# Kernel tuning notes

Measured on AMD Instinct MI355X. Metric: run time of the kernel, lower is better.

## Reference

```python
import jax, jax.numpy as jnp
import numpy as np

DT = 0.5
NE, NIN = 400, 784
# excitatory LIF
THRESH_E, OFFSET, VRESET_E, EREST_E, REFRAC_E, TAU_MEM_E = -52.0, 20.0, -65.0, -65.0, 5.0, 100.0
# inhibitory LIF
THRESH_I, VRESET_I, EREST_I, REFRAC_I, TAU_MEM_I = -40.0, -45.0, -60.0, 2.0, 10.0
# synapses
TAU_SYN_E, TAU_SYN_I = 1.0, 2.0
E_EI, E_IE, E_EE = 0.0, -100.0, 0.0
# STDP
TC_P1, TC_P2, TC_PRE = 20.0, 40.0, 20.0
NU_PRE, NU_POST, WMAX = 0.0001, 0.01, 1.0
THETA0 = 20.0


def lif_step(mem, rc, I, thresh, v_reset, erest, tau, refrac):
    # conductance-based LIF with refractory period (inferred LIFei semantics)
    active = rc <= 0.0
    mem = jnp.where(active, mem + (erest - mem + I) * (DT / tau), mem)
    rc = jnp.maximum(rc - DT, 0.0)
    spike = (active & (mem > thresh)).astype(mem.dtype)
    fired = spike > 0.0
    mem = jnp.where(fired, v_reset, mem)
    rc = jnp.where(fired, refrac, rc)
    return mem, rc, spike


def setup_inputs() -> dict:
    key = jax.random.key(0)
    k1, k2 = jax.random.split(key)
    x = jax.random.uniform(k1, (50, 512, NIN), dtype=jnp.float32)  # Poisson-rate encoded frames
    W_ine = (jax.random.uniform(k2, (NE, NIN), dtype=jnp.float32) + 0.01) * 0.3  # create_ine
    W_ei = jnp.eye(NE, dtype=jnp.float32) * 10.4                                  # create_ei
    W_ie = (jnp.ones((NE, NE), jnp.float32) - jnp.eye(NE, dtype=jnp.float32)) * 17.0  # create_ie
    return {"x": x, "W_ine": W_ine, "W_ei": W_ei, "W_ie": W_ie}


def reference(x, W_ine, W_ei, W_ie):
    T, B, _ = x.shape
    z_e = jnp.zeros((B, NE), x.dtype)

    def step(carry, xt_t):
        xt, t = xt_t
        (W, g_ine, g_ei, g_ie, Iie, mem_e, rc_e, mem_i, rc_i,
         theta, tr_pre, tp1, tp2) = carry
        # normweight: rows sum to 78.4
        W = W / (jnp.sum(W, axis=1, keepdims=True) / 78.4)
        # input -> e synapse (STDP-plastic)
        dg_ine = xt @ W.T                         # (B, NE)
        I_ine = g_ine * (E_EE - mem_e)            # g=0 at t=0 -> I=0 (matches None init)
        g_ine = g_ine + (dg_ine - g_ine) * (DT / TAU_SYN_E)
        # excitatory LIF with adaptive threshold
        thr_e = THRESH_E - OFFSET + theta
        mem_e, rc_e, spike_e = lif_step(mem_e, rc_e, I_ine + Iie, thr_e,
                                        VRESET_E, EREST_E, TAU_MEM_E, REFRAC_E)
        # e -> i synapse
        dg_ei = spike_e @ W_ei.T
        I_ei = g_ei * (E_EI - mem_i)
        g_ei = g_ei + (dg_ei - g_ei) * (DT / TAU_SYN_E)
        # inhibitory LIF
        mem_i, rc_i, spike_i = lif_step(mem_i, rc_i, I_ei, THRESH_I,
                                        VRESET_I, EREST_I, TAU_MEM_I, REFRAC_I)
        # i -> e synapse (current fed into NEXT step's lif_e)
        dg_ie = spike_i @ W_ie.T
        Iie = g_ie * (E_IE - mem_e)
        g_ie = g_ie + (dg_ie - g_ie) * (DT / TAU_SYN_I)
        # threshold homeostasis
        theta = theta * (1.0 - DT / 1e7) + 0.05 * spike_e
        # pre trace: first call copies x, later decay then set to 1 where x>0.9
        tr_pre_upd = jnp.where(xt > 0.9, 1.0, tr_pre * (1.0 - DT / TC_PRE))
        tr_pre = jnp.where(t == 0, xt, tr_pre_upd)
        # post traces: return decayed value, then set to 1 where spike
        ret1 = tp1 * (1.0 - DT / TC_P1)
        ret2 = tp2 * (1.0 - DT / TC_P2)
        fired = spike_e > 0.9
        tp1 = jnp.where(fired, 1.0, ret1)
        tp2 = jnp.where(fired, 1.0, ret2)
        # STDP: autograd.grad of dg=x@W^T w.r.t. W with grad_outputs G is G^T @ x
        dw = (NU_PRE * jnp.einsum('be,bi->ei', ret1, xt)
              + NU_POST * jnp.einsum('be,bi->ei', spike_e * ret2, tr_pre))
        W = jnp.clip(W + dw, 0.0, WMAX)
        new_carry = (W, g_ine, g_ei, g_ie, Iie, mem_e, rc_e, mem_i, rc_i,
                     theta, tr_pre, tp1, tp2)
        return new_carry, spike_e

    carry0 = (W_ine,
              z_e, z_e, z_e,                      # g_ine, g_ei, g_ie
              z_e,                                # Iie
              jnp.full((B, NE), EREST_E, x.dtype), z_e,   # mem_e, rc_e
              jnp.full((B, NE), EREST_I, x.dtype), z_e,   # mem_i, rc_i
              jnp.full((B, NE), THETA0, x.dtype),         # theta
              jnp.zeros((B, NIN), x.dtype),               # trace_pre
              z_e, z_e)                                   # trace_post1/2
    _, spikes = jax.lax.scan(step, carry0, (x, jnp.arange(T)))
    return spikes  # (T, B, NE)
```

## Files before the change

kernel.cpp:

```cpp
#include <hip/hip_runtime.h>

#define NE 400
#define NIN 784
#define BB 512
#define TT 50

#define KC1 7
#define KCH1 112
#define KC2 4
#define KCH2 128

constexpr float C_KE     = (float)(0.5 / 100.0);
constexpr float C_KI     = (float)(0.5 / 10.0);
constexpr float C_GSE    = 0.5f;
constexpr float C_GSI    = 0.25f;
constexpr float C_DECTH  = (float)(1.0 - 0.5 / 1e7);
constexpr float C_DEC1   = (float)(1.0 - 0.5 / 20.0);
constexpr float C_DEC2   = (float)(1.0 - 0.5 / 40.0);
constexpr float C_DECPRE = (float)(1.0 - 0.5 / 20.0);
constexpr float C_NUPRE  = (float)0.0001;
constexpr float C_NUPOST = 0.01f;

__global__ void k_init(float* g_ine, float* g_ei, float* g_ie, float* Iie,
                       float* mem_e, float* rc_e, float* mem_i, float* rc_i,
                       float* theta, float* tp1, float* tp2) {
    int i = blockIdx.x * blockDim.x + threadIdx.x;
    if (i < BB * NE) {
        g_ine[i] = 0.f; g_ei[i] = 0.f; g_ie[i] = 0.f; Iie[i] = 0.f;
        mem_e[i] = -65.0f; rc_e[i] = 0.f;
        mem_i[i] = -60.0f; rc_i[i] = 0.f;
        theta[i] = 20.0f; tp1[i] = 0.f; tp2[i] = 0.f;
    }
}

__global__ __launch_bounds__(256) void k_rowsum0(const float* __restrict__ W,
                                                 float* __restrict__ d) {
    int e = blockIdx.x, tid = threadIdx.x;
    __shared__ float red[256];
    float s = 0.f;
    if (tid < 196) {
        float4 w = *(const float4*)&W[e * NIN + tid * 4];
        s = w.x + w.y + w.z + w.w;
    }
    red[tid] = s;
    __syncthreads();
    for (int off = 128; off > 0; off >>= 1) {
        if (tid < off) red[tid] += red[tid + off];
        __syncthreads();
    }
    if (tid == 0) d[e] = red[0] / 78.4f;
}

__global__ __launch_bounds__(256) void k_gemm1(const float* __restrict__ x,
                                               const float* __restrict__ W,
                                               float* __restrict__ dgp) {
    __shared__ float xs[16][68];
    __shared__ float ws[16][68];
    int tx = threadIdx.x & 15, ty = threadIdx.x >> 4;
    int lid = threadIdx.x;
    int e0 = blockIdx.x * 64, b0 = blockIdx.y * 64;
    int kbase = blockIdx.z * KCH1;

    float acc[4][4];
#pragma unroll
    for (int r = 0; r < 4; r++)
#pragma unroll
        for (int c = 0; c < 4; c++) acc[r][c] = 0.f;

    for (int kt = 0; kt < KCH1; kt += 16) {
        int k0 = kbase + kt;
        {
            int r = lid >> 2, cb = (lid & 3) * 4;
            float4 xv = *(const float4*)&x[(b0 + r) * NIN + k0 + cb];
            xs[cb + 0][r] = xv.x; xs[cb + 1][r] = xv.y;
            xs[cb + 2][r] = xv.z; xs[cb + 3][r] = xv.w;
            float4 wv;
            if (e0 + r < NE) wv = *(const float4*)&W[(e0 + r) * NIN + k0 + cb];
            else wv = make_float4(0.f, 0.f, 0.f, 0.f);
            ws[cb + 0][r] = wv.x; ws[cb + 1][r] = wv.y;
            ws[cb + 2][r] = wv.z; ws[cb + 3][r] = wv.w;
        }
        __syncthreads();
#pragma unroll
        for (int k = 0; k < 16; k++) {
            float4 av = *(const float4*)&xs[k][ty * 4];
            float4 bv = *(const float4*)&ws[k][tx * 4];
            float a[4] = {av.x, av.y, av.z, av.w};
            float b[4] = {bv.x, bv.y, bv.z, bv.w};
#pragma unroll
            for (int r = 0; r < 4; r++)
#pragma unroll
                for (int c = 0; c < 4; c++) acc[r][c] += a[r] * b[c];
        }
        __syncthreads();
    }
    if (e0 + tx * 4 < NE) {
        float* base = dgp + (size_t)blockIdx.z * BB * NE;
#pragma unroll
        for (int r = 0; r < 4; r++) {
            float4 v = make_float4(acc[r][0], acc[r][1], acc[r][2], acc[r][3]);
            *(float4*)&base[(b0 + ty * 4 + r) * NE + e0 + tx * 4] = v;
        }
    }
}

__global__ __launch_bounds__(512) void k_mid(const float* __restrict__ dgp,
                                             const float* __restrict__ d,
                                             const float* __restrict__ xt,
                                             float* __restrict__ tr, int t,
                                             float* g_ine, float* g_ei, float* g_ie,
                                             float* Iie, float* mem_e, float* rc_e,
                                             float* mem_i, float* rc_i, float* theta,
                                             float* tp1, float* tp2,
                                             float* __restrict__ A1,
                                             float* __restrict__ A2,
                                             float* __restrict__ out_t) {
    if (blockIdx.x >= BB) {
        int base = (blockIdx.x - BB) * 2048 + threadIdx.x * 4;
        float4 xv = *(const float4*)&xt[base];
        float4 o;
        if (t == 0) {
            o = xv;
        } else {
            float4 tv = *(const float4*)&tr[base];
            o.x = (xv.x > 0.9f) ? 1.0f : tv.x * C_DECPRE;
            o.y = (xv.y > 0.9f) ? 1.0f : tv.y * C_DECPRE;
            o.z = (xv.z > 0.9f) ? 1.0f : tv.z * C_DECPRE;
            o.w = (xv.w > 0.9f) ? 1.0f : tv.w * C_DECPRE;
        }
        *(float4*)&tr[base] = o;
        return;
    }
    int b = blockIdx.x;
    int e = threadIdx.x;
    __shared__ float red[512];
    int idx = b * NE + e;

    float spk_i = 0.f, spk_e = 0.f;
    float g1 = 0.f, me = 0.f, re = 0.f, th = 0.f, g2 = 0.f, mi = 0.f, ri = 0.f;

    if (e < NE) {
        float dg = 0.f;
#pragma unroll
        for (int c = 0; c < KC1; c++) dg += dgp[(size_t)c * BB * NE + idx];
        dg = dg / d[e];
        g1 = g_ine[idx]; me = mem_e[idx]; re = rc_e[idx];
        th = theta[idx];
        float Ii = Iie[idx];
        float I_in = g1 * (0.0f - me);
        g1 = g1 + (dg - g1) * C_GSE;
        bool act = (re <= 0.0f);
        float I = I_in + Ii;
        if (act) me = me + ((-65.0f - me) + I) * C_KE;
        re = fmaxf(re - 0.5f, 0.0f);
        float thr = -72.0f + th;
        spk_e = (act && (me > thr)) ? 1.0f : 0.0f;
        if (spk_e > 0.0f) { me = -65.0f; re = 5.0f; }
        float dgei = spk_e * 10.4f;
        g2 = g_ei[idx]; mi = mem_i[idx]; ri = rc_i[idx];
        float I_ei = g2 * (0.0f - mi);
        g2 = g2 + (dgei - g2) * C_GSE;
        bool ai = (ri <= 0.0f);
        if (ai) mi = mi + ((-60.0f - mi) + I_ei) * C_KI;
        ri = fmaxf(ri - 0.5f, 0.0f);
        spk_i = (ai && (mi > -40.0f)) ? 1.0f : 0.0f;
        if (spk_i > 0.0f) { mi = -45.0f; ri = 2.0f; }
    }
    red[e] = spk_i;
    __syncthreads();
    for (int off = 256; off > 0; off >>= 1) {
        if (e < off) red[e] += red[e + off];
        __syncthreads();
    }
    float S = red[0];
    if (e < NE) {
        float dgie = 17.0f * (S - spk_i);
        float g3 = g_ie[idx];
        float Iie_new = g3 * (-100.0f - me);
        g3 = g3 + (dgie - g3) * C_GSI;
        th = th * C_DECTH + 0.05f * spk_e;
        float r1 = tp1[idx] * C_DEC1;
        float r2 = tp2[idx] * C_DEC2;
        bool fired = spk_e > 0.9f;
        A1[idx] = r1;
        A2[idx] = spk_e * r2;
        tp1[idx] = fired ? 1.0f : r1;
        tp2[idx] = fired ? 1.0f : r2;
        g_ine[idx] = g1; g_ei[idx] = g2; g_ie[idx] = g3; Iie[idx] = Iie_new;
        mem_e[idx] = me; rc_e[idx] = re; mem_i[idx] = mi; rc_i[idx] = ri;
        theta[idx] = th;
        out_t[idx] = spk_e;
    }
}

__global__ __launch_bounds__(256) void k_gemm2(const float* __restrict__ A1,
                                               const float* __restrict__ A2,
                                               const float* __restrict__ xt,
                                               const float* __restrict__ tr,
                                               float* __restrict__ part) {
    __shared__ float a1s[16][68];
    __shared__ float a2s[16][68];
    __shared__ float xs[16][68];
    __shared__ float ts[16][68];
    int tx = threadIdx.x & 15, ty = threadIdx.x >> 4;
    int lid = threadIdx.x;
    int i0 = blockIdx.x * 64, e0 = blockIdx.y * 64;
    int bbase = blockIdx.z * KCH2;

    float s1[4][4], s2[4][4];
#pragma unroll
    for (int r = 0; r < 4; r++)
#pragma unroll
        for (int c = 0; c < 4; c++) { s1[r][c] = 0.f; s2[r][c] = 0.f; }

    for (int bt = 0; bt < KCH2; bt += 16) {
        int b0 = bbase + bt;
        {
            int r = lid >> 4, cb = (lid & 15) * 4;
            float4 v1, v2;
            if (e0 + cb < NE) {
                v1 = *(const float4*)&A1[(b0 + r) * NE + e0 + cb];
                v2 = *(const float4*)&A2[(b0 + r) * NE + e0 + cb];
            } else {
                v1 = make_float4(0.f, 0.f, 0.f, 0.f);
                v2 = v1;
            }
            *(float4*)&a1s[r][cb] = v1;
            *(float4*)&a2s[r][cb] = v2;
            float4 xv, tv;
            if (i0 + cb < NIN) {
                xv = *(const float4*)&xt[(b0 + r) * NIN + i0 + cb];
                tv = *(const float4*)&tr[(b0 + r) * NIN + i0 + cb];
            } else {
                xv = make_float4(0.f, 0.f, 0.f, 0.f);
                tv = xv;
            }
            *(float4*)&xs[r][cb] = xv;
            *(float4*)&ts[r][cb] = tv;
        }
        __syncthreads();
#pragma unroll
        for (int k = 0; k < 16; k++) {
            float4 a1v = *(const float4*)&a1s[k][ty * 4];
            float4 a2v = *(const float4*)&a2s[k][ty * 4];
            float4 xv = *(const float4*)&xs[k][tx * 4];
            float4 tv = *(const float4*)&ts[k][tx * 4];
            float a1[4] = {a1v.x, a1v.y, a1v.z, a1v.w};
            float a2[4] = {a2v.x, a2v.y, a2v.z, a2v.w};
            float xx[4] = {xv.x, xv.y, xv.z, xv.w};
            float tt[4] = {tv.x, tv.y, tv.z, tv.w};
#pragma unroll
            for (int r = 0; r < 4; r++)
#pragma unroll
                for (int c = 0; c < 4; c++) {
                    s1[r][c] += a1[r] * xx[c];
                    s2[r][c] += a2[r] * tt[c];
                }
        }
        __syncthreads();
    }
    if (e0 + ty * 4 < NE && i0 + tx * 4 < NIN) {
        float* base = part + (size_t)blockIdx.z * NE * NIN;
#pragma unroll
        for (int r = 0; r < 4; r++) {
            float4 v = make_float4(C_NUPRE * s1[r][0] + C_NUPOST * s2[r][0],
                                   C_NUPRE * s1[r][1] + C_NUPOST * s2[r][1],
                                   C_NUPRE * s1[r][2] + C_NUPOST * s2[r][2],
                                   C_NUPRE * s1[r][3] + C_NUPOST * s2[r][3]);
            *(float4*)&base[(e0 + ty * 4 + r) * NIN + i0 + tx * 4] = v;
        }
    }
}

__global__ __launch_bounds__(256) void k_wupdate(float* __restrict__ W,
                                                 const float* __restrict__ part,
                                                 float* __restrict__ d) {
    int e = blockIdx.x, tid = threadIdx.x;
    __shared__ float red[256];
    float dv = d[e];
    float s = 0.f;
    if (tid < 196) {
        int off = e * NIN + tid * 4;
        float4 w = *(const float4*)&W[off];
        float4 acc = make_float4(w.x / dv, w.y / dv, w.z / dv, w.w / dv);
#pragma unroll
        for (int c = 0; c < KC2; c++) {
            float4 p = *(const float4*)&part[(size_t)c * NE * NIN + off];
            acc.x += p.x; acc.y += p.y; acc.z += p.z; acc.w += p.w;
        }
        acc.x = fminf(fmaxf(acc.x, 0.f), 1.f);
        acc.y = fminf(fmaxf(acc.y, 0.f), 1.f);
        acc.z = fminf(fmaxf(acc.z, 0.f), 1.f);
        acc.w = fminf(fmaxf(acc.w, 0.f), 1.f);
        *(float4*)&W[off] = acc;
        s = acc.x + acc.y + acc.z + acc.w;
    }
    red[tid] = s;
    __syncthreads();
    for (int off = 128; off > 0; off >>= 1) {
        if (tid < off) red[tid] += red[tid + off];
        __syncthreads();
    }
    if (tid == 0) d[e] = red[0] / 78.4f;
}

extern "C" void kernel_launch(void* const* d_in, const int* in_sizes, int n_in,
                              void* d_out, int out_size, void* d_ws, size_t ws_size,
                              hipStream_t stream) {
    const float* x     = (const float*)d_in[0];
    const float* W_ine = (const float*)d_in[1];

    float* p = (float*)d_ws;
    float* W_cur = p; p += NE * NIN;
    float* dbuf  = p; p += NE;
    float* dgp   = p; p += (size_t)KC1 * BB * NE;
    float* part  = p; p += (size_t)KC2 * NE * NIN;
    float* A1    = p; p += BB * NE;
    float* A2    = p; p += BB * NE;
    float* g_ine = p; p += BB * NE;
    float* g_ei  = p; p += BB * NE;
    float* g_ie  = p; p += BB * NE;
    float* Iie   = p; p += BB * NE;
    float* mem_e = p; p += BB * NE;
    float* rc_e  = p; p += BB * NE;
    float* mem_i = p; p += BB * NE;
    float* rc_i  = p; p += BB * NE;
    float* theta = p; p += BB * NE;
    float* tp1   = p; p += BB * NE;
    float* tp2   = p; p += BB * NE;
    float* tr    = p; p += BB * NIN;

    hipMemcpyAsync(W_cur, W_ine, (size_t)NE * NIN * sizeof(float),
                   hipMemcpyDeviceToDevice, stream);
    k_init<<<(BB * NE + 255) / 256, 256, 0, stream>>>(g_ine, g_ei, g_ie, Iie, mem_e,
                                                      rc_e, mem_i, rc_i, theta, tp1, tp2);
    k_rowsum0<<<NE, 256, 0, stream>>>(W_cur, dbuf);

    for (int t = 0; t < TT; t++) {
        const float* xt = x + (size_t)t * BB * NIN;
        float* out_t = (float*)d_out + (size_t)t * BB * NE;
        k_gemm1<<<dim3(7, 8, KC1), 256, 0, stream>>>(xt, W_cur, dgp);
        k_mid<<<BB + 196, 512, 0, stream>>>(dgp, dbuf, xt, tr, t, g_ine, g_ei, g_ie,
                                            Iie, mem_e, rc_e, mem_i, rc_i, theta,
                                            tp1, tp2, A1, A2, out_t);
        k_gemm2<<<dim3(13, 7, KC2), 256, 0, stream>>>(A1, A2, xt, tr, part);
        k_wupdate<<<NE, 256, 0, stream>>>(W_cur, part, dbuf);
    }
}
```

Baseline: 2.607 ms.

## Retile both GEMMs with register prefetch, fold STDP GEMM, skip final update

Both GEMMs now use 64x128 output tiles with register-level prefetch of the next k-slice, so the global-memory load overlaps the shared-memory FMA loop. The two STDP outer products are merged into one GEMM over a concatenated 2B reduction dimension, with NU_PRE and NU_POST pre-applied in k_mid, and the split-K count is doubled. The inhibitory-spike reduction uses wavefront shuffles in place of a shared-memory tree. The weight-update GEMM is skipped on the last timestep because its result is never read. Larger tiles raise register pressure and reduce the number of blocks.

```diff
diff --git a/kernel.cpp b/kernel.cpp
--- a/kernel.cpp
+++ b/kernel.cpp
@@ -7,7 +7,7 @@
 
 #define KC1 7
 #define KCH1 112
-#define KC2 4
+#define KC2 8
 #define KCH2 128
 
 constexpr float C_KE     = (float)(0.5 / 100.0);
@@ -51,56 +51,75 @@
     if (tid == 0) d[e] = red[0] / 78.4f;
 }
 
-__global__ __launch_bounds__(256) void k_gemm1(const float* __restrict__ x,
-                                               const float* __restrict__ W,
-                                               float* __restrict__ dgp) {
-    __shared__ float xs[16][68];
-    __shared__ float ws[16][68];
-    int tx = threadIdx.x & 15, ty = threadIdx.x >> 4;
-    int lid = threadIdx.x;
-    int e0 = blockIdx.x * 64, b0 = blockIdx.y * 64;
-    int kbase = blockIdx.z * KCH1;
-
-    float acc[4][4];
-#pragma unroll
-    for (int r = 0; r < 4; r++)
-#pragma unroll
-        for (int c = 0; c < 4; c++) acc[r][c] = 0.f;
-
-    for (int kt = 0; kt < KCH1; kt += 16) {
-        int k0 = kbase + kt;
-        {
-            int r = lid >> 2, cb = (lid & 3) * 4;
-            float4 xv = *(const float4*)&x[(b0 + r) * NIN + k0 + cb];
-            xs[cb + 0][r] = xv.x; xs[cb + 1][r] = xv.y;
-            xs[cb + 2][r] = xv.z; xs[cb + 3][r] = xv.w;
-            float4 wv;
-            if (e0 + r < NE) wv = *(const float4*)&W[(e0 + r) * NIN + k0 + cb];
-            else wv = make_float4(0.f, 0.f, 0.f, 0.f);
-            ws[cb + 0][r] = wv.x; ws[cb + 1][r] = wv.y;
-            ws[cb + 2][r] = wv.z; ws[cb + 3][r] = wv.w;
-        }
-        __syncthreads();
+__global__ __launch_bounds__(256) void k_g1(const float* __restrict__ x,
+                                            const float* __restrict__ W,
+                                            float* __restrict__ dgp) {
+    __shared__ float sA[16][68];
+    __shared__ float sB[16][132];
+    const int lid = threadIdx.x;
+    const int tx = lid & 15, ty = lid >> 4;
+    const int e0 = blockIdx.x * 128, b0 = blockIdx.y * 64;
+    const int kb = blockIdx.z * KCH1;
+    const int sr = lid >> 2;
+    const int sj = (lid & 3) * 4;
+    const float4 z4 = make_float4(0.f, 0.f, 0.f, 0.f);
+
+    float acc[4][2][4];
+#pragma unroll
+    for (int p = 0; p < 4; p++)
+#pragma unroll
+        for (int h = 0; h < 2; h++)
+#pragma unroll
+            for (int q = 0; q < 4; q++) acc[p][h][q] = 0.f;
+
+    float4 xv, wv0, wv1;
+    auto ld = [&](int kt) {
+        int k0 = kb + kt * 16;
+        xv = *(const float4*)&x[(b0 + sr) * NIN + k0 + sj];
+        int e1 = e0 + sr, e2 = e0 + 64 + sr;
+        wv0 = (e1 < NE) ? *(const float4*)&W[e1 * NIN + k0 + sj] : z4;
+        wv1 = (e2 < NE) ? *(const float4*)&W[e2 * NIN + k0 + sj] : z4;
+    };
+
+    ld(0);
+    for (int kt = 0; kt < KCH1 / 16; kt++) {
+        sA[sj + 0][sr] = xv.x; sA[sj + 1][sr] = xv.y;
+        sA[sj + 2][sr] = xv.z; sA[sj + 3][sr] = xv.w;
+        sB[sj + 0][sr] = wv0.x; sB[sj + 1][sr] = wv0.y;
+        sB[sj + 2][sr] = wv0.z; sB[sj + 3][sr] = wv0.w;
+        sB[sj + 0][64 + sr] = wv1.x; sB[sj + 1][64 + sr] = wv1.y;
+        sB[sj + 2][64 + sr] = wv1.z; sB[sj + 3][64 + sr] = wv1.w;
+        __syncthreads();
+        if (kt < KCH1 / 16 - 1) ld(kt + 1);
 #pragma unroll
         for (int k = 0; k < 16; k++) {
-            float4 av = *(const float4*)&xs[k][ty * 4];
-            float4 bv = *(const float4*)&ws[k][tx * 4];
+            float4 av = *(const float4*)&sA[k][ty * 4];
+            float4 b0v = *(const float4*)&sB[k][tx * 4];
+            float4 b1v = *(const float4*)&sB[k][64 + tx * 4];
             float a[4] = {av.x, av.y, av.z, av.w};
-            float b[4] = {bv.x, bv.y, bv.z, bv.w};
-#pragma unroll
-            for (int r = 0; r < 4; r++)
-#pragma unroll
-                for (int c = 0; c < 4; c++) acc[r][c] += a[r] * b[c];
-        }
-        __syncthreads();
-    }
-    if (e0 + tx * 4 < NE) {
-        float* base = dgp + (size_t)blockIdx.z * BB * NE;
-#pragma unroll
-        for (int r = 0; r < 4; r++) {
-            float4 v = make_float4(acc[r][0], acc[r][1], acc[r][2], acc[r][3]);
-            *(float4*)&base[(b0 + ty * 4 + r) * NE + e0 + tx * 4] = v;
-        }
+            float bq0[4] = {b0v.x, b0v.y, b0v.z, b0v.w};
+            float bq1[4] = {b1v.x, b1v.y, b1v.z, b1v.w};
+#pragma unroll
+            for (int p = 0; p < 4; p++)
+#pragma unroll
+                for (int q = 0; q < 4; q++) {
+                    acc[p][0][q] += a[p] * bq0[q];
+                    acc[p][1][q] += a[p] * bq1[q];
+                }
+        }
+        __syncthreads();
+    }
+    float* basep = dgp + (size_t)blockIdx.z * BB * NE;
+    int c1 = e0 + tx * 4, c2 = e0 + 64 + tx * 4;
+#pragma unroll
+    for (int p = 0; p < 4; p++) {
+        int row = b0 + ty * 4 + p;
+        if (c1 < NE)
+            *(float4*)&basep[row * NE + c1] =
+                make_float4(acc[p][0][0], acc[p][0][1], acc[p][0][2], acc[p][0][3]);
+        if (c2 < NE)
+            *(float4*)&basep[row * NE + c2] =
+                make_float4(acc[p][1][0], acc[p][1][1], acc[p][1][2], acc[p][1][3]);
     }
 }
 
@@ -112,8 +131,8 @@
                                              float* Iie, float* mem_e, float* rc_e,
                                              float* mem_i, float* rc_i, float* theta,
                                              float* tp1, float* tp2,
-                                             float* __restrict__ A1,
-                                             float* __restrict__ A2,
+                                             float* __restrict__ A1s,
+                                             float* __restrict__ A2s,
                                              float* __restrict__ out_t) {
     if (blockIdx.x >= BB) {
         int base = (blockIdx.x - BB) * 2048 + threadIdx.x * 4;
@@ -123,17 +142,17 @@
             o = xv;
         } else {
             float4 tv = *(const float4*)&tr[base];
-            o.x = (xv.x > 0.9f) ? 1.0f : tv.x * C_DECPRE;
-            o.y = (xv.y > 0.9f) ? 1.0f : tv.y * C_DECPRE;
-            o.z = (xv.z > 0.9f) ? 1.0f : tv.z * C_DECPRE;
-            o.w = (xv.w > 0.9f) ? 1.0f : tv.w * C_DECPRE;
+            o.x = (xv.x > 0.9f) ? 1.f : tv.x * C_DECPRE;
+            o.y = (xv.y > 0.9f) ? 1.f : tv.y * C_DECPRE;
+            o.z = (xv.z > 0.9f) ? 1.f : tv.z * C_DECPRE;
+            o.w = (xv.w > 0.9f) ? 1.f : tv.w * C_DECPRE;
         }
         *(float4*)&tr[base] = o;
         return;
     }
     int b = blockIdx.x;
     int e = threadIdx.x;
-    __shared__ float red[512];
+    __shared__ float red[8];
     int idx = b * NE + e;
 
     float spk_i = 0.f, spk_e = 0.f;
@@ -166,115 +185,115 @@
         spk_i = (ai && (mi > -40.0f)) ? 1.0f : 0.0f;
         if (spk_i > 0.0f) { mi = -45.0f; ri = 2.0f; }
     }
-    red[e] = spk_i;
+    float v = spk_i;
+#pragma unroll
+    for (int o = 32; o > 0; o >>= 1) v += __shfl_down(v, o, 64);
+    if ((e & 63) == 0) red[e >> 6] = v;
     __syncthreads();
-    for (int off = 256; off > 0; off >>= 1) {
-        if (e < off) red[e] += red[e + off];
-        __syncthreads();
-    }
-    float S = red[0];
+    float S = ((red[0] + red[1]) + (red[2] + red[3])) +
+              ((red[4] + red[5]) + (red[6] + red[7]));
     if (e < NE) {
         float dgie = 17.0f * (S - spk_i);
         float g3 = g_ie[idx];
         float Iie_new = g3 * (-100.0f - me);
         g3 = g3 + (dgie - g3) * C_GSI;
-        th = th * C_DECTH + 0.05f * spk_e;
+        float th2 = th * C_DECTH + 0.05f * spk_e;
         float r1 = tp1[idx] * C_DEC1;
         float r2 = tp2[idx] * C_DEC2;
         bool fired = spk_e > 0.9f;
-        A1[idx] = r1;
-        A2[idx] = spk_e * r2;
+        A1s[idx] = C_NUPRE * r1;
+        A2s[idx] = C_NUPOST * (spk_e * r2);
         tp1[idx] = fired ? 1.0f : r1;
         tp2[idx] = fired ? 1.0f : r2;
         g_ine[idx] = g1; g_ei[idx] = g2; g_ie[idx] = g3; Iie[idx] = Iie_new;
         mem_e[idx] = me; rc_e[idx] = re; mem_i[idx] = mi; rc_i[idx] = ri;
-        theta[idx] = th;
+        theta[idx] = th2;
         out_t[idx] = spk_e;
     }
 }
 
-__global__ __launch_bounds__(256) void k_gemm2(const float* __restrict__ A1,
-                                               const float* __restrict__ A2,
-                                               const float* __restrict__ xt,
-                                               const float* __restrict__ tr,
-                                               float* __restrict__ part) {
-    __shared__ float a1s[16][68];
-    __shared__ float a2s[16][68];
-    __shared__ float xs[16][68];
-    __shared__ float ts[16][68];
-    int tx = threadIdx.x & 15, ty = threadIdx.x >> 4;
-    int lid = threadIdx.x;
-    int i0 = blockIdx.x * 64, e0 = blockIdx.y * 64;
-    int bbase = blockIdx.z * KCH2;
-
-    float s1[4][4], s2[4][4];
-#pragma unroll
-    for (int r = 0; r < 4; r++)
-#pragma unroll
-        for (int c = 0; c < 4; c++) { s1[r][c] = 0.f; s2[r][c] = 0.f; }
-
-    for (int bt = 0; bt < KCH2; bt += 16) {
-        int b0 = bbase + bt;
-        {
-            int r = lid >> 4, cb = (lid & 15) * 4;
-            float4 v1, v2;
-            if (e0 + cb < NE) {
-                v1 = *(const float4*)&A1[(b0 + r) * NE + e0 + cb];
-                v2 = *(const float4*)&A2[(b0 + r) * NE + e0 + cb];
-            } else {
-                v1 = make_float4(0.f, 0.f, 0.f, 0.f);
-                v2 = v1;
-            }
-            *(float4*)&a1s[r][cb] = v1;
-            *(float4*)&a2s[r][cb] = v2;
-            float4 xv, tv;
-            if (i0 + cb < NIN) {
-                xv = *(const float4*)&xt[(b0 + r) * NIN + i0 + cb];
-                tv = *(const float4*)&tr[(b0 + r) * NIN + i0 + cb];
-            } else {
-                xv = make_float4(0.f, 0.f, 0.f, 0.f);
-                tv = xv;
-            }
-            *(float4*)&xs[r][cb] = xv;
-            *(float4*)&ts[r][cb] = tv;
-        }
-        __syncthreads();
+__global__ __launch_bounds__(256) void k_g2(const float* __restrict__ A1s,
+                                            const float* __restrict__ A2s,
+                                            const float* __restrict__ x,
+                                            const float* __restrict__ tr,
+                                            float* __restrict__ part) {
+    __shared__ float sA[16][68];
+    __shared__ float sB[16][132];
+    const int lid = threadIdx.x;
+    const int tx = lid & 15, ty = lid >> 4;
+    const int e0 = blockIdx.x * 64, i0 = blockIdx.y * 128;
+    const int kb = blockIdx.z * KCH2;
+    const int kr = lid >> 4;
+    const int jc = (lid & 15) * 4;
+    const float4 z4 = make_float4(0.f, 0.f, 0.f, 0.f);
+
+    float acc[4][2][4];
+#pragma unroll
+    for (int p = 0; p < 4; p++)
+#pragma unroll
+        for (int h = 0; h < 2; h++)
+#pragma unroll
+            for (int q = 0; q < 4; q++) acc[p][h][q] = 0.f;
+
+    float4 av_, bv0_, bv1_;
+    auto ld = [&](int kt) {
+        int gb = kb + kt * 16 + kr;
+        int ec = e0 + jc;
+        if (ec < NE)
+            av_ = (gb < BB) ? *(const float4*)&A1s[gb * NE + ec]
+                            : *(const float4*)&A2s[(gb - BB) * NE + ec];
+        else av_ = z4;
+        const float* src; int rb;
+        if (gb < BB) { src = x; rb = gb; } else { src = tr; rb = gb - BB; }
+        int c1 = i0 + jc, c2 = i0 + 64 + jc;
+        bv0_ = (c1 < NIN) ? *(const float4*)&src[rb * NIN + c1] : z4;
+        bv1_ = (c2 < NIN) ? *(const float4*)&src[rb * NIN + c2] : z4;
+    };
+
+    ld(0);
+    for (int kt = 0; kt < KCH2 / 16; kt++) {
+        *(float4*)&sA[kr][jc] = av_;
+        *(float4*)&sB[kr][jc] = bv0_;
+        *(float4*)&sB[kr][64 + jc] = bv1_;
+        __syncthreads();
+        if (kt < KCH2 / 16 - 1) ld(kt + 1);
 #pragma unroll
         for (int k = 0; k < 16; k++) {
-            float4 a1v = *(const float4*)&a1s[k][ty * 4];
-            float4 a2v = *(const float4*)&a2s[k][ty * 4];
-            float4 xv = *(const float4*)&xs[k][tx * 4];
-            float4 tv = *(const float4*)&ts[k][tx * 4];
-            float a1[4] = {a1v.x, a1v.y, a1v.z, a1v.w};
-            float a2[4] = {a2v.x, a2v.y, a2v.z, a2v.w};
-            float xx[4] = {xv.x, xv.y, xv.z, xv.w};
-            float tt[4] = {tv.x, tv.y, tv.z, tv.w};
-#pragma unroll
-            for (int r = 0; r < 4; r++)
-#pragma unroll
-                for (int c = 0; c < 4; c++) {
-                    s1[r][c] += a1[r] * xx[c];
-                    s2[r][c] += a2[r] * tt[c];
+            float4 av = *(const float4*)&sA[k][ty * 4];
+            float4 b0v = *(const float4*)&sB[k][tx * 4];
+            float4 b1v = *(const float4*)&sB[k][64 + tx * 4];
+            float a[4] = {av.x, av.y, av.z, av.w};
+            float bq0[4] = {b0v.x, b0v.y, b0v.z, b0v.w};
+            float bq1[4] = {b1v.x, b1v.y, b1v.z, b1v.w};
+#pragma unroll
+            for (int p = 0; p < 4; p++)
+#pragma unroll
+                for (int q = 0; q < 4; q++) {
+                    acc[p][0][q] += a[p] * bq0[q];
+                    acc[p][1][q] += a[p] * bq1[q];
                 }
         }
         __syncthreads();
     }
-    if (e0 + ty * 4 < NE && i0 + tx * 4 < NIN) {
-        float* base = part + (size_t)blockIdx.z * NE * NIN;
-#pragma unroll
-        for (int r = 0; r < 4; r++) {
-            float4 v = make_float4(C_NUPRE * s1[r][0] + C_NUPOST * s2[r][0],
-                                   C_NUPRE * s1[r][1] + C_NUPOST * s2[r][1],
-                                   C_NUPRE * s1[r][2] + C_NUPOST * s2[r][2],
-                                   C_NUPRE * s1[r][3] + C_NUPOST * s2[r][3]);
-            *(float4*)&base[(e0 + ty * 4 + r) * NIN + i0 + tx * 4] = v;
-        }
-    }
-}
-
-__global__ __launch_bounds__(256) void k_wupdate(float* __restrict__ W,
-                                                 const float* __restrict__ part,
-                                                 float* __restrict__ d) {
+    float* basep = part + (size_t)blockIdx.z * NE * NIN;
+    int c1 = i0 + tx * 4, c2 = i0 + 64 + tx * 4;
+#pragma unroll
+    for (int p = 0; p < 4; p++) {
+        int row = e0 + ty * 4 + p;
+        if (row < NE) {
+            if (c1 < NIN)
+                *(float4*)&basep[row * NIN + c1] =
+                    make_float4(acc[p][0][0], acc[p][0][1], acc[p][0][2], acc[p][0][3]);
+            if (c2 < NIN)
+                *(float4*)&basep[row * NIN + c2] =
+                    make_float4(acc[p][1][0], acc[p][1][1], acc[p][1][2], acc[p][1][3]);
+        }
+    }
+}
+
+__global__ __launch_bounds__(256) void k_wup(float* __restrict__ W,
+                                             const float* __restrict__ part,
+                                             float* __restrict__ d) {
     int e = blockIdx.x, tid = threadIdx.x;
     __shared__ float red[256];
     float dv = d[e];
@@ -315,8 +334,8 @@
     float* dbuf  = p; p += NE;
     float* dgp   = p; p += (size_t)KC1 * BB * NE;
     float* part  = p; p += (size_t)KC2 * NE * NIN;
-    float* A1    = p; p += BB * NE;
-    float* A2    = p; p += BB * NE;
+    float* A1s   = p; p += BB * NE;
+    float* A2s   = p; p += BB * NE;
     float* g_ine = p; p += BB * NE;
     float* g_ei  = p; p += BB * NE;
     float* g_ie  = p; p += BB * NE;
@@ -339,11 +358,13 @@
     for (int t = 0; t < TT; t++) {
         const float* xt = x + (size_t)t * BB * NIN;
         float* out_t = (float*)d_out + (size_t)t * BB * NE;
-        k_gemm1<<<dim3(7, 8, KC1), 256, 0, stream>>>(xt, W_cur, dgp);
+        k_g1<<<dim3(4, 8, KC1), 256, 0, stream>>>(xt, W_cur, dgp);
         k_mid<<<BB + 196, 512, 0, stream>>>(dgp, dbuf, xt, tr, t, g_ine, g_ei, g_ie,
                                             Iie, mem_e, rc_e, mem_i, rc_i, theta,
-                                            tp1, tp2, A1, A2, out_t);
-        k_gemm2<<<dim3(13, 7, KC2), 256, 0, stream>>>(A1, A2, xt, tr, part);
-        k_wupdate<<<NE, 256, 0, stream>>>(W_cur, part, dbuf);
-    }
-}
+                                            tp1, tp2, A1s, A2s, out_t);
+        if (t < TT - 1) {
+            k_g2<<<dim3(7, 7, KC2), 256, 0, stream>>>(A1s, A2s, xt, tr, part);
+            k_wup<<<NE, 256, 0, stream>>>(W_cur, part, dbuf);
+        }
+    }
+}
```

After: 2.232 ms. 14.4% less time.
